# Performance work log

Measured on AMD Instinct MI355X. Metric: run time of the kernel, lower is better.

## Reference

```python
import jax, jax.numpy as jnp
import numpy as np

B, Q, K, H = 16, 512, 512, 64
DQ, DK, DV = 256, 256, 256
MASK_VAL = -1000000.0


def setup_inputs() -> dict:
    key = jax.random.key(0)
    ks = jax.random.split(key, 7)
    queries = jax.random.normal(ks[0], (B, Q, DQ), dtype=jnp.float32)
    keys = jax.random.normal(ks[1], (B, K, DK), dtype=jnp.float32)
    values = jax.random.normal(ks[2], (B, K, DV), dtype=jnp.float32)
    valid_lens = jax.random.randint(ks[3], (B,), 1, K + 1).astype(jnp.int32)
    # learned params (nn.Linear, bias=False): weight shape [out, in]
    Wq = jax.random.normal(ks[4], (H, DQ), dtype=jnp.float32) / np.sqrt(DQ)
    Wk = jax.random.normal(ks[5], (H, DK), dtype=jnp.float32) / np.sqrt(DK)
    wv = jax.random.normal(ks[6], (H,), dtype=jnp.float32) / np.sqrt(H)
    return {"queries": queries, "keys": keys, "values": values,
            "valid_lens": valid_lens, "Wq": Wq, "Wk": Wk, "wv": wv}


def reference(queries, keys, values, valid_lens, Wq, Wk, wv):
    q = jnp.einsum('bqd,hd->bqh', queries, Wq)          # [B,Q,H]
    k = jnp.einsum('bkd,hd->bkh', keys, Wk)             # [B,K,H]
    feats = jnp.tanh(q[:, :, None, :] + k[:, None, :, :])  # [B,Q,K,H]
    scores = jnp.einsum('bqkh,h->bqk', feats, wv)       # [B,Q,K]
    kmask = jnp.arange(K)[None, None, :] < valid_lens[:, None, None]
    scores = jnp.where(kmask, scores, MASK_VAL)
    attn = jax.nn.softmax(scores, axis=-1)              # [B,Q,K]
    return jnp.einsum('bqk,bkv->bqv', attn, values)     # [B,Q,DV]
```

## Files before the change

kernel.cpp:

```cpp
#include <hip/hip_runtime.h>
#include <math.h>

#if defined(__has_builtin)
#  if __has_builtin(__builtin_amdgcn_exp2f)
#    define EXP2F(x) __builtin_amdgcn_exp2f(x)
#  endif
#  if __has_builtin(__builtin_amdgcn_rcpf)
#    define RCPF(x) __builtin_amdgcn_rcpf(x)
#  endif
#endif
#ifndef EXP2F
#  define EXP2F(x) exp2f(x)
#endif
#ifndef RCPF
#  define RCPF(x) (1.0f/(x))
#endif

static constexpr int Bn = 16, QN = 512, KN = 512, Hn = 64, DV = 256, DIN = 256;
static constexpr int TQ = 8;
static constexpr float TWO_LOG2E = 2.8853900817779268f;
static constexpr float LOG2E     = 1.4426950408889634f;

typedef __attribute__((ext_vector_type(8))) short short8;
typedef __attribute__((ext_vector_type(4))) float f32x4;

__device__ __forceinline__ short f2bf(float x) {
  unsigned u = __builtin_bit_cast(unsigned, x);
  u += 0x7FFF + ((u >> 16) & 1);
  return (short)(u >> 16);
}
__device__ __forceinline__ float bf2f(short h) {
  return __builtin_bit_cast(float, ((unsigned)(unsigned short)h) << 16);
}

__global__ __launch_bounds__(256) void prep_kernel(
    const float* __restrict__ Wq, const float* __restrict__ Wk,
    ushort* __restrict__ wqh, ushort* __restrict__ wql,
    ushort* __restrict__ wkh, ushort* __restrict__ wkl)
{
  int i = blockIdx.x * 256 + threadIdx.x;
  float xq = Wq[i];
  short hq = f2bf(xq);
  wqh[i] = (ushort)hq; wql[i] = (ushort)f2bf(xq - bf2f(hq));
  float xk = Wk[i];
  short hk = f2bf(xk);
  wkh[i] = (ushort)hk; wkl[i] = (ushort)f2bf(xk - bf2f(hk));
}

__global__ __launch_bounds__(256) void proj_mfma(
    const float* __restrict__ queries, const float* __restrict__ keys,
    const ushort* __restrict__ wqh, const ushort* __restrict__ wql,
    const ushort* __restrict__ wkh, const ushort* __restrict__ wkl,
    float* __restrict__ qe, float* __restrict__ ekT)
{
  int t = threadIdx.x;
  int lane = t & 63, wid = t >> 6;
  int tile = blockIdx.x * 2 + (wid >> 1);
  int nhalf = wid & 1;
  bool is_k = tile >= 512;
  int trow = (tile & 511) * 16;
  const float*  X  = is_k ? keys : queries;
  const ushort* Wh = is_k ? wkh : wqh;
  const ushort* Wl = is_k ? wkl : wql;
  int mr = lane & 15, quad = lane >> 4;
  const float* xp = X + (size_t)(trow + mr) * DIN + quad * 8;
  int coln = nhalf * 32 + mr;
  const ushort* whp = Wh + (size_t)coln * DIN + quad * 8;
  const ushort* wlp = Wl + (size_t)coln * DIN + quad * 8;

  f32x4 acc[2];
  acc[0] = (f32x4){0.f, 0.f, 0.f, 0.f};
  acc[1] = (f32x4){0.f, 0.f, 0.f, 0.f};

  #pragma unroll
  for (int kc = 0; kc < 8; ++kc) {
    float4 a0 = *(const float4*)(xp + kc * 32);
    float4 a1 = *(const float4*)(xp + kc * 32 + 4);
    float av[8] = {a0.x, a0.y, a0.z, a0.w, a1.x, a1.y, a1.z, a1.w};
    short8 ah, al;
    #pragma unroll
    for (int j = 0; j < 8; ++j) {
      ah[j] = f2bf(av[j]);
      al[j] = f2bf(av[j] - bf2f(ah[j]));
    }
    #pragma unroll
    for (int nt = 0; nt < 2; ++nt) {
      short8 bh = *(const short8*)(whp + (size_t)nt * 16 * DIN + kc * 32);
      short8 bl = *(const short8*)(wlp + (size_t)nt * 16 * DIN + kc * 32);
      acc[nt] = __builtin_amdgcn_mfma_f32_16x16x32_bf16(al, bh, acc[nt], 0, 0, 0);
      acc[nt] = __builtin_amdgcn_mfma_f32_16x16x32_bf16(ah, bl, acc[nt], 0, 0, 0);
      acc[nt] = __builtin_amdgcn_mfma_f32_16x16x32_bf16(ah, bh, acc[nt], 0, 0, 0);
    }
  }
  #pragma unroll
  for (int nt = 0; nt < 2; ++nt) {
    int col = nhalf * 32 + nt * 16 + mr;
    #pragma unroll
    for (int reg = 0; reg < 4; ++reg) {
      int row = trow + quad * 4 + reg;
      int b = row >> 9, r = row & (QN - 1);
      float e = EXP2F(acc[nt][reg] * TWO_LOG2E);
      if (!is_k) qe[((size_t)b * QN + r) * Hn + col] = e;
      else       ekT[((size_t)b * Hn + col) * KN + r] = e;
    }
  }
}

__global__ __launch_bounds__(256, 4) void attn_kernel(
    const float* __restrict__ qe,
    const float* __restrict__ ekT,
    const float* __restrict__ values,
    const int*   __restrict__ valid_lens,
    const float* __restrict__ wv,
    float* __restrict__ out)
{
  __shared__ __align__(16) float qes2[Hn][TQ];
  __shared__ __align__(16) float pt[KN][TQ];
  __shared__ float wsum[4][TQ];
  __shared__ float inv_s[TQ];

  int t = threadIdx.x;
  int b = blockIdx.x >> 6;
  int q0 = (blockIdx.x & 63) * TQ;
  int L = valid_lens[b];
  int lane = t & 63, wave = t >> 6;

  {
    int i0 = t, i1 = t + 256;
    qes2[i0 >> 3][i0 & 7] = qe[((size_t)b * QN + q0 + (i0 & 7)) * Hn + (i0 >> 3)];
    qes2[i1 >> 3][i1 & 7] = qe[((size_t)b * QN + q0 + (i1 & 7)) * Hn + (i1 >> 3)];
  }
  __syncthreads();

  float S = 0.f;
  #pragma unroll
  for (int h = 0; h < Hn; ++h) S += wv[h];

  float rowsum[TQ];
  #pragma unroll
  for (int r = 0; r < TQ; ++r) rowsum[r] = 0.f;
  #pragma unroll
  for (int j = 0; j < 2; ++j) {
    int k = t + j * 256;
    if (k < L) {
      float sc[TQ];
      #pragma unroll
      for (int r = 0; r < TQ; ++r) sc[r] = S;
      const float* kbase = ekT + (size_t)b * Hn * KN + k;
      #pragma unroll 2
      for (int h = 0; h < Hn; ++h) {
        float ek = kbase[(size_t)h * KN];
        float4 qa = *(const float4*)&qes2[h][0];
        float4 qb = *(const float4*)&qes2[h][4];
        float w2 = 2.0f * wv[h];
        sc[0] -= w2 * RCPF(qa.x * ek + 1.0f);
        sc[1] -= w2 * RCPF(qa.y * ek + 1.0f);
        sc[2] -= w2 * RCPF(qa.z * ek + 1.0f);
        sc[3] -= w2 * RCPF(qa.w * ek + 1.0f);
        sc[4] -= w2 * RCPF(qb.x * ek + 1.0f);
        sc[5] -= w2 * RCPF(qb.y * ek + 1.0f);
        sc[6] -= w2 * RCPF(qb.z * ek + 1.0f);
        sc[7] -= w2 * RCPF(qb.w * ek + 1.0f);
      }
      float p[TQ];
      #pragma unroll
      for (int r = 0; r < TQ; ++r) { p[r] = EXP2F(sc[r] * LOG2E); rowsum[r] += p[r]; }
      *(float4*)&pt[k][0] = make_float4(p[0], p[1], p[2], p[3]);
      *(float4*)&pt[k][4] = make_float4(p[4], p[5], p[6], p[7]);
    }
  }
  #pragma unroll
  for (int r = 0; r < TQ; ++r) {
    float s = rowsum[r];
    #pragma unroll
    for (int off = 32; off > 0; off >>= 1) s += __shfl_xor(s, off, 64);
    if (lane == r) wsum[wave][r] = s;
  }
  __syncthreads();
  if (t < TQ) {
    float s = wsum[0][t] + wsum[1][t] + wsum[2][t] + wsum[3][t];
    inv_s[t] = 1.0f / s;
  }
  __syncthreads();

  float acc[TQ];
  #pragma unroll
  for (int r = 0; r < TQ; ++r) acc[r] = 0.f;
  const float* vb = values + (size_t)b * KN * DV + t;
  #pragma unroll 2
  for (int k = 0; k < L; ++k) {
    float val = vb[(size_t)k * DV];
    float4 pa = *(const float4*)&pt[k][0];
    float4 pb = *(const float4*)&pt[k][4];
    acc[0] += pa.x * val; acc[1] += pa.y * val;
    acc[2] += pa.z * val; acc[3] += pa.w * val;
    acc[4] += pb.x * val; acc[5] += pb.y * val;
    acc[6] += pb.z * val; acc[7] += pb.w * val;
  }
  float* ob = out + ((size_t)b * QN + q0) * DV + t;
  #pragma unroll
  for (int r = 0; r < TQ; ++r) ob[(size_t)r * DV] = acc[r] * inv_s[r];
}

extern "C" void kernel_launch(void* const* d_in, const int* in_sizes, int n_in,
                              void* d_out, int out_size, void* d_ws, size_t ws_size,
                              hipStream_t stream) {
  const float* queries    = (const float*)d_in[0];
  const float* keys       = (const float*)d_in[1];
  const float* values     = (const float*)d_in[2];
  const int*   valid_lens = (const int*)d_in[3];
  const float* Wq         = (const float*)d_in[4];
  const float* Wk         = (const float*)d_in[5];
  const float* wv         = (const float*)d_in[6];
  float* out = (float*)d_out;

  char* ws = (char*)d_ws;
  float*  qe  = (float*)ws;
  float*  ekT = qe + (size_t)Bn * QN * Hn;
  ushort* wqh = (ushort*)(ekT + (size_t)Bn * Hn * KN);
  ushort* wql = wqh + Hn * DIN;
  ushort* wkh = wql + Hn * DIN;
  ushort* wkl = wkh + Hn * DIN;

  prep_kernel<<<64, 256, 0, stream>>>(Wq, Wk, wqh, wql, wkh, wkl);
  proj_mfma<<<512, 256, 0, stream>>>(queries, keys, wqh, wql, wkh, wkl, qe, ekT);
  attn_kernel<<<Bn * (QN / TQ), 256, 0, stream>>>(qe, ekT, values,
                                                  valid_lens, wv, out);
}
```

Measured before the change: 171.1 us.

## Fuse prep, projection and attention into one cooperative kernel with grid sync

Merges the three launches into one cooperative kernel of 1024 blocks of 512 threads, separated by grid-wide barriers, with a fallback to three launches if the cooperative launch fails. It also moves to 512-thread blocks: each attention thread handles one key, the PV loop is split in two halves over keys and reduced through shared memory, and projection writes the transposed key tiles through a shared staging buffer so stores are coalesced. The aim is to remove launch gaps and raise parallelism per block. The risk is that 1024 blocks of 512 threads must all be co-resident for the grid sync, plus the barrier cost itself.

```diff
diff --git a/kernel.cpp b/kernel.cpp
--- a/kernel.cpp
+++ b/kernel.cpp
@@ -1,5 +1,8 @@
 #include <hip/hip_runtime.h>
+#include <hip/hip_cooperative_groups.h>
 #include <math.h>
+
+namespace cg = cooperative_groups;
 
 #if defined(__has_builtin)
 #  if __has_builtin(__builtin_amdgcn_exp2f)
@@ -33,12 +36,20 @@
   return __builtin_bit_cast(float, ((unsigned)(unsigned short)h) << 16);
 }
 
-__global__ __launch_bounds__(256) void prep_kernel(
-    const float* __restrict__ Wq, const float* __restrict__ Wk,
-    ushort* __restrict__ wqh, ushort* __restrict__ wql,
-    ushort* __restrict__ wkh, ushort* __restrict__ wkl)
-{
-  int i = blockIdx.x * 256 + threadIdx.x;
+struct AttnS {
+  float qes2[Hn][TQ];
+  float pt[KN][12];
+  float pacc[TQ][DV];
+  float wsum[8][TQ];
+  float inv_s[TQ];
+};
+struct ProjS { float tr[8][16][20]; };
+
+__device__ __forceinline__ void prep_phase(
+    int blk, int t, const float* Wq, const float* Wk,
+    ushort* wqh, ushort* wql, ushort* wkh, ushort* wkl)
+{
+  int i = blk * 512 + t;
   float xq = Wq[i];
   short hq = f2bf(xq);
   wqh[i] = (ushort)hq; wql[i] = (ushort)f2bf(xq - bf2f(hq));
@@ -47,31 +58,28 @@
   wkh[i] = (ushort)hk; wkl[i] = (ushort)f2bf(xk - bf2f(hk));
 }
 
-__global__ __launch_bounds__(256) void proj_mfma(
-    const float* __restrict__ queries, const float* __restrict__ keys,
-    const ushort* __restrict__ wqh, const ushort* __restrict__ wql,
-    const ushort* __restrict__ wkh, const ushort* __restrict__ wkl,
-    float* __restrict__ qe, float* __restrict__ ekT)
-{
-  int t = threadIdx.x;
+__device__ __forceinline__ void proj_phase(
+    char* smem, int blk, int t,
+    const float* queries, const float* keys,
+    const ushort* wqh, const ushort* wql,
+    const ushort* wkh, const ushort* wkl,
+    float* qe, float* ekT)
+{
+  ProjS& P = *reinterpret_cast<ProjS*>(smem);
   int lane = t & 63, wid = t >> 6;
-  int tile = blockIdx.x * 2 + (wid >> 1);
-  int nhalf = wid & 1;
+  int sub = wid >> 2, wid4 = wid & 3;
+  int tile = blk * 2 + sub;
   bool is_k = tile >= 512;
   int trow = (tile & 511) * 16;
   const float*  X  = is_k ? keys : queries;
   const ushort* Wh = is_k ? wkh : wqh;
   const ushort* Wl = is_k ? wkl : wql;
   int mr = lane & 15, quad = lane >> 4;
-  const float* xp = X + (size_t)(trow + mr) * DIN + quad * 8;
-  int coln = nhalf * 32 + mr;
-  const ushort* whp = Wh + (size_t)coln * DIN + quad * 8;
-  const ushort* wlp = Wl + (size_t)coln * DIN + quad * 8;
-
-  f32x4 acc[2];
-  acc[0] = (f32x4){0.f, 0.f, 0.f, 0.f};
-  acc[1] = (f32x4){0.f, 0.f, 0.f, 0.f};
-
+  const float*  xp  = X  + (size_t)(trow + mr) * DIN + quad * 8;
+  const ushort* whp = Wh + (size_t)(wid4 * 16 + mr) * DIN + quad * 8;
+  const ushort* wlp = Wl + (size_t)(wid4 * 16 + mr) * DIN + quad * 8;
+
+  f32x4 acc = (f32x4){0.f, 0.f, 0.f, 0.f};
   #pragma unroll
   for (int kc = 0; kc < 8; ++kc) {
     float4 a0 = *(const float4*)(xp + kc * 32);
@@ -83,123 +91,175 @@
       ah[j] = f2bf(av[j]);
       al[j] = f2bf(av[j] - bf2f(ah[j]));
     }
-    #pragma unroll
-    for (int nt = 0; nt < 2; ++nt) {
-      short8 bh = *(const short8*)(whp + (size_t)nt * 16 * DIN + kc * 32);
-      short8 bl = *(const short8*)(wlp + (size_t)nt * 16 * DIN + kc * 32);
-      acc[nt] = __builtin_amdgcn_mfma_f32_16x16x32_bf16(al, bh, acc[nt], 0, 0, 0);
-      acc[nt] = __builtin_amdgcn_mfma_f32_16x16x32_bf16(ah, bl, acc[nt], 0, 0, 0);
-      acc[nt] = __builtin_amdgcn_mfma_f32_16x16x32_bf16(ah, bh, acc[nt], 0, 0, 0);
-    }
-  }
-  #pragma unroll
-  for (int nt = 0; nt < 2; ++nt) {
-    int col = nhalf * 32 + nt * 16 + mr;
+    short8 bh = *(const short8*)(whp + kc * 32);
+    short8 bl = *(const short8*)(wlp + kc * 32);
+    acc = __builtin_amdgcn_mfma_f32_16x16x32_bf16(al, bh, acc, 0, 0, 0);
+    acc = __builtin_amdgcn_mfma_f32_16x16x32_bf16(ah, bl, acc, 0, 0, 0);
+    acc = __builtin_amdgcn_mfma_f32_16x16x32_bf16(ah, bh, acc, 0, 0, 0);
+  }
+  if (!is_k) {
     #pragma unroll
     for (int reg = 0; reg < 4; ++reg) {
       int row = trow + quad * 4 + reg;
-      int b = row >> 9, r = row & (QN - 1);
-      float e = EXP2F(acc[nt][reg] * TWO_LOG2E);
-      if (!is_k) qe[((size_t)b * QN + r) * Hn + col] = e;
-      else       ekT[((size_t)b * Hn + col) * KN + r] = e;
-    }
-  }
-}
-
-__global__ __launch_bounds__(256, 4) void attn_kernel(
-    const float* __restrict__ qe,
-    const float* __restrict__ ekT,
-    const float* __restrict__ values,
-    const int*   __restrict__ valid_lens,
-    const float* __restrict__ wv,
-    float* __restrict__ out)
-{
-  __shared__ __align__(16) float qes2[Hn][TQ];
-  __shared__ __align__(16) float pt[KN][TQ];
-  __shared__ float wsum[4][TQ];
-  __shared__ float inv_s[TQ];
-
-  int t = threadIdx.x;
-  int b = blockIdx.x >> 6;
-  int q0 = (blockIdx.x & 63) * TQ;
+      qe[(size_t)row * Hn + wid4 * 16 + mr] = EXP2F(acc[reg] * TWO_LOG2E);
+    }
+  } else {
+    #pragma unroll
+    for (int reg = 0; reg < 4; ++reg)
+      P.tr[wid][mr][quad * 4 + reg] = EXP2F(acc[reg] * TWO_LOG2E);
+    int b = trow >> 9, kr = trow & (KN - 1);
+    #pragma unroll
+    for (int hp = 0; hp < 4; ++hp) {
+      int h_l = hp * 4 + quad, k_l = mr;
+      ekT[((size_t)b * Hn + wid4 * 16 + h_l) * KN + kr + k_l] = P.tr[wid][h_l][k_l];
+    }
+  }
+}
+
+__device__ __forceinline__ void attn_phase(
+    char* smem, int blk, int t,
+    const float* qe, const float* ekT, const float* values,
+    const int* valid_lens, const float* wv, float* out)
+{
+  AttnS& S = *reinterpret_cast<AttnS*>(smem);
+  int b = blk >> 6;
+  int q0 = (blk & 63) * TQ;
   int L = valid_lens[b];
   int lane = t & 63, wave = t >> 6;
 
+  S.qes2[t >> 3][t & 7] = qe[(size_t)(b * QN + q0 + (t & 7)) * Hn + (t >> 3)];
+  __syncthreads();
+
+  float Ssum = 0.f;
+  #pragma unroll
+  for (int h = 0; h < Hn; ++h) Ssum += wv[h];
+
   {
-    int i0 = t, i1 = t + 256;
-    qes2[i0 >> 3][i0 & 7] = qe[((size_t)b * QN + q0 + (i0 & 7)) * Hn + (i0 >> 3)];
-    qes2[i1 >> 3][i1 & 7] = qe[((size_t)b * QN + q0 + (i1 & 7)) * Hn + (i1 >> 3)];
-  }
-  __syncthreads();
-
-  float S = 0.f;
-  #pragma unroll
-  for (int h = 0; h < Hn; ++h) S += wv[h];
-
-  float rowsum[TQ];
-  #pragma unroll
-  for (int r = 0; r < TQ; ++r) rowsum[r] = 0.f;
-  #pragma unroll
-  for (int j = 0; j < 2; ++j) {
-    int k = t + j * 256;
+    int k = t;
+    float p[TQ];
     if (k < L) {
       float sc[TQ];
       #pragma unroll
-      for (int r = 0; r < TQ; ++r) sc[r] = S;
-      const float* kbase = ekT + (size_t)b * Hn * KN + k;
-      #pragma unroll 2
-      for (int h = 0; h < Hn; ++h) {
-        float ek = kbase[(size_t)h * KN];
-        float4 qa = *(const float4*)&qes2[h][0];
-        float4 qb = *(const float4*)&qes2[h][4];
-        float w2 = 2.0f * wv[h];
-        sc[0] -= w2 * RCPF(qa.x * ek + 1.0f);
-        sc[1] -= w2 * RCPF(qa.y * ek + 1.0f);
-        sc[2] -= w2 * RCPF(qa.z * ek + 1.0f);
-        sc[3] -= w2 * RCPF(qa.w * ek + 1.0f);
-        sc[4] -= w2 * RCPF(qb.x * ek + 1.0f);
-        sc[5] -= w2 * RCPF(qb.y * ek + 1.0f);
-        sc[6] -= w2 * RCPF(qb.z * ek + 1.0f);
-        sc[7] -= w2 * RCPF(qb.w * ek + 1.0f);
+      for (int r = 0; r < TQ; ++r) sc[r] = Ssum;
+      const float* kb = ekT + (size_t)b * Hn * KN + k;
+      for (int h0 = 0; h0 < Hn; h0 += 8) {
+        float ekv[8];
+        #pragma unroll
+        for (int j = 0; j < 8; ++j)
+          ekv[j] = kb[(size_t)(h0 + j) * KN];
+        #pragma unroll
+        for (int j = 0; j < 8; ++j) {
+          int h = h0 + j;
+          float w2 = 2.0f * wv[h];
+          float4 qa = *(const float4*)&S.qes2[h][0];
+          float4 qb = *(const float4*)&S.qes2[h][4];
+          float ek = ekv[j];
+          sc[0] -= w2 * RCPF(qa.x * ek + 1.0f);
+          sc[1] -= w2 * RCPF(qa.y * ek + 1.0f);
+          sc[2] -= w2 * RCPF(qa.z * ek + 1.0f);
+          sc[3] -= w2 * RCPF(qa.w * ek + 1.0f);
+          sc[4] -= w2 * RCPF(qb.x * ek + 1.0f);
+          sc[5] -= w2 * RCPF(qb.y * ek + 1.0f);
+          sc[6] -= w2 * RCPF(qb.z * ek + 1.0f);
+          sc[7] -= w2 * RCPF(qb.w * ek + 1.0f);
+        }
       }
-      float p[TQ];
-      #pragma unroll
-      for (int r = 0; r < TQ; ++r) { p[r] = EXP2F(sc[r] * LOG2E); rowsum[r] += p[r]; }
-      *(float4*)&pt[k][0] = make_float4(p[0], p[1], p[2], p[3]);
-      *(float4*)&pt[k][4] = make_float4(p[4], p[5], p[6], p[7]);
-    }
-  }
-  #pragma unroll
-  for (int r = 0; r < TQ; ++r) {
-    float s = rowsum[r];
-    #pragma unroll
-    for (int off = 32; off > 0; off >>= 1) s += __shfl_xor(s, off, 64);
-    if (lane == r) wsum[wave][r] = s;
+      #pragma unroll
+      for (int r = 0; r < TQ; ++r) p[r] = EXP2F(sc[r] * LOG2E);
+      *(float4*)&S.pt[k][0] = make_float4(p[0], p[1], p[2], p[3]);
+      *(float4*)&S.pt[k][4] = make_float4(p[4], p[5], p[6], p[7]);
+    } else {
+      #pragma unroll
+      for (int r = 0; r < TQ; ++r) p[r] = 0.f;
+    }
+    #pragma unroll
+    for (int r = 0; r < TQ; ++r) {
+      float s = p[r];
+      #pragma unroll
+      for (int off = 32; off > 0; off >>= 1) s += __shfl_xor(s, off, 64);
+      if (lane == r) S.wsum[wave][r] = s;
+    }
   }
   __syncthreads();
   if (t < TQ) {
-    float s = wsum[0][t] + wsum[1][t] + wsum[2][t] + wsum[3][t];
-    inv_s[t] = 1.0f / s;
-  }
-  __syncthreads();
-
+    float s = 0.f;
+    #pragma unroll
+    for (int w = 0; w < 8; ++w) s += S.wsum[w][t];
+    S.inv_s[t] = 1.0f / s;
+  }
+
+  int c = t & (DV - 1), half = t >> 8;
+  int mid = L >> 1;
+  int k0 = half ? mid : 0;
+  int k1 = half ? L : mid;
   float acc[TQ];
   #pragma unroll
   for (int r = 0; r < TQ; ++r) acc[r] = 0.f;
-  const float* vb = values + (size_t)b * KN * DV + t;
-  #pragma unroll 2
-  for (int k = 0; k < L; ++k) {
+  const float* vb = values + (size_t)b * KN * DV + c;
+  #pragma unroll 4
+  for (int k = k0; k < k1; ++k) {
     float val = vb[(size_t)k * DV];
-    float4 pa = *(const float4*)&pt[k][0];
-    float4 pb = *(const float4*)&pt[k][4];
+    float4 pa = *(const float4*)&S.pt[k][0];
+    float4 pb = *(const float4*)&S.pt[k][4];
     acc[0] += pa.x * val; acc[1] += pa.y * val;
     acc[2] += pa.z * val; acc[3] += pa.w * val;
     acc[4] += pb.x * val; acc[5] += pb.y * val;
     acc[6] += pb.z * val; acc[7] += pb.w * val;
   }
-  float* ob = out + ((size_t)b * QN + q0) * DV + t;
-  #pragma unroll
-  for (int r = 0; r < TQ; ++r) ob[(size_t)r * DV] = acc[r] * inv_s[r];
+  if (half) {
+    #pragma unroll
+    for (int r = 0; r < TQ; ++r) S.pacc[r][c] = acc[r];
+  }
+  __syncthreads();
+  if (!half) {
+    float* ob = out + (size_t)(b * QN + q0) * DV + c;
+    #pragma unroll
+    for (int r = 0; r < TQ; ++r)
+      ob[(size_t)r * DV] = (acc[r] + S.pacc[r][c]) * S.inv_s[r];
+  }
+}
+
+__global__ __launch_bounds__(512, 8) void mega_kernel(
+    const float* queries, const float* keys, const float* values,
+    const int* valid_lens, const float* Wq, const float* Wk, const float* wv,
+    ushort* wqh, ushort* wql, ushort* wkh, ushort* wkl,
+    float* qe, float* ekT, float* out)
+{
+  __shared__ __align__(16) char smem[sizeof(AttnS)];
+  cg::grid_group grid = cg::this_grid();
+  int t = threadIdx.x, blk = blockIdx.x;
+
+  if (blk < 32) prep_phase(blk, t, Wq, Wk, wqh, wql, wkh, wkl);
+  grid.sync();
+  if (blk < 512)
+    proj_phase(smem, blk, t, queries, keys, wqh, wql, wkh, wkl, qe, ekT);
+  grid.sync();
+  attn_phase(smem, blk, t, qe, ekT, values, valid_lens, wv, out);
+}
+
+__global__ __launch_bounds__(512) void prep_k(
+    const float* Wq, const float* Wk,
+    ushort* wqh, ushort* wql, ushort* wkh, ushort* wkl)
+{
+  prep_phase(blockIdx.x, threadIdx.x, Wq, Wk, wqh, wql, wkh, wkl);
+}
+__global__ __launch_bounds__(512) void proj_k(
+    const float* queries, const float* keys,
+    const ushort* wqh, const ushort* wql,
+    const ushort* wkh, const ushort* wkl,
+    float* qe, float* ekT)
+{
+  __shared__ __align__(16) char smem[sizeof(ProjS)];
+  proj_phase(smem, blockIdx.x, threadIdx.x, queries, keys,
+             wqh, wql, wkh, wkl, qe, ekT);
+}
+__global__ __launch_bounds__(512) void attn_k(
+    const float* qe, const float* ekT, const float* values,
+    const int* valid_lens, const float* wv, float* out)
+{
+  __shared__ __align__(16) char smem[sizeof(AttnS)];
+  attn_phase(smem, blockIdx.x, threadIdx.x, qe, ekT, values,
+             valid_lens, wv, out);
 }
 
 extern "C" void kernel_launch(void* const* d_in, const int* in_sizes, int n_in,
@@ -222,8 +282,17 @@
   ushort* wkh = wql + Hn * DIN;
   ushort* wkl = wkh + Hn * DIN;
 
-  prep_kernel<<<64, 256, 0, stream>>>(Wq, Wk, wqh, wql, wkh, wkl);
-  proj_mfma<<<512, 256, 0, stream>>>(queries, keys, wqh, wql, wkh, wkl, qe, ekT);
-  attn_kernel<<<Bn * (QN / TQ), 256, 0, stream>>>(qe, ekT, values,
-                                                  valid_lens, wv, out);
-}
+  void* args[] = {
+    (void*)&queries, (void*)&keys, (void*)&values, (void*)&valid_lens,
+    (void*)&Wq, (void*)&Wk, (void*)&wv,
+    (void*)&wqh, (void*)&wql, (void*)&wkh, (void*)&wkl,
+    (void*)&qe, (void*)&ekT, (void*)&out,
+  };
+  hipError_t err = hipLaunchCooperativeKernel(
+      (const void*)mega_kernel, dim3(1024), dim3(512), args, 0, stream);
+  if (err != hipSuccess) {
+    prep_k<<<32, 512, 0, stream>>>(Wq, Wk, wqh, wql, wkh, wkl);
+    proj_k<<<512, 512, 0, stream>>>(queries, keys, wqh, wql, wkh, wkl, qe, ekT);
+    attn_k<<<1024, 512, 0, stream>>>(qe, ekT, values, valid_lens, wv, out);
+  }
+}
```

New measurement: 409.9 us. +139.5%, slower.
